# Kernel optimization log

Hardware: AMD Instinct MI355X
Metric: run time of the kernel (lower is better)

Reference implementation:

```python
import jax, jax.numpy as jnp
import numpy as np

N_NODES = 100000
N_EDGES = 1600000
N_GRAPHS = 128
IN_DIM, HID, OUT_DIM, DOC_DIM = 64, 128, 32, 768
LAYERS = 3


def setup_inputs() -> dict:
    key = jax.random.key(0)
    ks = jax.random.split(key, 24)
    s = 0.05
    inp = {
        "x": jax.random.normal(ks[0], (N_NODES, IN_DIM), jnp.float32),
        "doc_features": jax.random.normal(ks[1], (N_GRAPHS, DOC_DIM), jnp.float32),
        "edge_index": jax.random.randint(ks[2], (2, N_EDGES), 0, N_NODES, jnp.int64),
        "batch": jnp.sort(jax.random.randint(ks[3], (N_NODES,), 0, N_GRAPHS, jnp.int64)),
        # parameters (stored as [in, out] so y = x @ W + b)
        "node_w": jax.random.normal(ks[4], (IN_DIM, HID), jnp.float32) * s,
        "node_b": jnp.zeros((HID,), jnp.float32),
        "ggnn_w": jax.random.normal(ks[5], (LAYERS, HID, HID), jnp.float32) * s,
        "gru_w_ih": jax.random.normal(ks[6], (HID, 3 * HID), jnp.float32) * s,
        "gru_b_ih": jnp.zeros((3 * HID,), jnp.float32),
        "gru_w_hh": jax.random.normal(ks[7], (HID, 3 * HID), jnp.float32) * s,
        "gru_b_hh": jnp.zeros((3 * HID,), jnp.float32),
        "doc_w": jax.random.normal(ks[8], (DOC_DIM, HID), jnp.float32) * s,
        "doc_b": jnp.zeros((HID,), jnp.float32),
        "ln_g": jnp.ones((2 * HID,), jnp.float32),
        "ln_b": jnp.zeros((2 * HID,), jnp.float32),
        "fus_w": jax.random.normal(ks[9], (2 * HID, HID), jnp.float32) * s,
        "fus_b": jnp.zeros((HID,), jnp.float32),
        "task_w": jax.random.normal(ks[10], (HID, OUT_DIM), jnp.float32) * s,
        "task_b": jnp.zeros((OUT_DIM,), jnp.float32),
        "time_w": jax.random.normal(ks[11], (HID, 1), jnp.float32) * s,
        "time_b": jnp.zeros((1,), jnp.float32),
    }
    return inp


def _gru(m, h, w_ih, b_ih, w_hh, b_hh):
    gi = m @ w_ih + b_ih  # [N, 3H]
    gh = h @ w_hh + b_hh
    ir, iz, in_ = jnp.split(gi, 3, axis=-1)
    hr, hz, hn = jnp.split(gh, 3, axis=-1)
    r = jax.nn.sigmoid(ir + hr)
    z = jax.nn.sigmoid(iz + hz)
    n = jnp.tanh(in_ + r * hn)
    return (1.0 - z) * n + z * h


def reference(x, doc_features, node_w, node_b, ggnn_w, gru_w_ih, gru_b_ih,
              gru_w_hh, gru_b_hh, doc_w, doc_b, ln_g, ln_b, fus_w, fus_b,
              task_w, task_b, time_w, time_b, edge_index, batch):
    N = x.shape[0]
    src, dst = edge_index[0], edge_index[1]
    # node projection + ReLU
    h = jax.nn.relu(x @ node_w + node_b)  # [N, H]
    # GatedGraphConv: 3 layers of (linear -> scatter-add over edges -> GRU)
    for i in range(LAYERS):
        m = h @ ggnn_w[i]                              # [N, H]
        agg = jax.ops.segment_sum(m[src], dst, num_segments=N)  # scatter-add
        h = _gru(agg, h, gru_w_ih, gru_b_ih, gru_w_hh, gru_b_hh)
    # global mean pool over graphs
    sums = jax.ops.segment_sum(h, batch, num_segments=N_GRAPHS)  # [G, H]
    cnt = jax.ops.segment_sum(jnp.ones((N,), h.dtype), batch, num_segments=N_GRAPHS)
    pooled = sums / jnp.maximum(cnt, 1.0)[:, None]
    # doc projection + fusion head
    doc_emb = jax.nn.relu(doc_features @ doc_w + doc_b)  # [G, H]
    fusion = jnp.concatenate([pooled, doc_emb], axis=1)  # [G, 2H]
    mu = jnp.mean(fusion, axis=-1, keepdims=True)
    var = jnp.mean(jnp.square(fusion - mu), axis=-1, keepdims=True)
    fusion = (fusion - mu) * jax.lax.rsqrt(var + 1e-5) * ln_g + ln_b
    fusion = jax.nn.relu(fusion @ fus_w + fus_b)  # dropout is identity (eval)
    task_output = fusion @ task_w + task_b
    time_output = fusion @ time_w + time_b
    return (task_output, time_output)
```

## Files before the change

### kernel.cpp

```cpp
#include <hip/hip_runtime.h>

#define N_NODES  100000
#define N_EDGES  1600000
#define N_GRAPHS 128

#define BSH      8
#define BNODES   (1 << BSH)
#define NBUCK    391
#define NBLK_P1  512
#define EPB      (N_EDGES / NBLK_P1)
#define BKT_SCAN_N   (NBUCK * NBLK_P1)
#define SCAN_BLK_BKT 196
#define SCAN_BLK_NODE 98

typedef unsigned short u16;
typedef unsigned int   u32;
typedef __attribute__((ext_vector_type(8))) short short8;
typedef __attribute__((ext_vector_type(4))) float f32x4;

__device__ __forceinline__ float bf2f(u16 v) {
  union { u32 i; float f; } u; u.i = ((u32)v) << 16; return u.f;
}
__device__ __forceinline__ u16 f2bf(float f) {
  union { float f; u32 i; } u; u.f = f;
  u32 r = (u.i + 0x7fffu + ((u.i >> 16) & 1u)) >> 16;
  return (u16)r;
}
__device__ __forceinline__ float sigmoid_f(float x) { return 1.f / (1.f + __expf(-x)); }
__device__ __forceinline__ float tanh_f(float x) {
  x = fminf(15.f, fmaxf(-15.f, x));
  float e = __expf(2.f * x);
  return (e - 1.f) / (e + 1.f);
}
__device__ __forceinline__ int geti(const int* __restrict__ p, int i, int is64) {
  return p[is64 ? (2 * i) : i];
}

__global__ void detect_i64_kernel(const int* __restrict__ ei, const int* __restrict__ batch,
                                  int* __restrict__ flags) {
  int lane = threadIdx.x;
  {
    long long q = (long long)lane * (3200000 / 2 - 1) / 63;
    int pos = (int)(2 * q + 1);
    unsigned long long m = __ballot(ei[pos] != 0);
    if (lane == 0) flags[0] = (m == 0ull) ? 1 : 0;
  }
  {
    long long q = (long long)lane * (100000 / 2 - 1) / 63;
    int pos = (int)(2 * q + 1);
    unsigned long long m = __ballot(batch[pos] != 0);
    if (lane == 0) flags[1] = (m == 0ull) ? 1 : 0;
  }
}


__global__ __launch_bounds__(256)
void bucket_hist(const int* __restrict__ ei, const int* __restrict__ flags,
                 int* __restrict__ bcounts) {
  __shared__ int h[NBUCK];
  const int f = flags[0];
  for (int b = threadIdx.x; b < NBUCK; b += 256) h[b] = 0;
  __syncthreads();
  const int e0 = blockIdx.x * EPB;
  for (int i = threadIdx.x; i < EPB; i += 256) {
    int d = geti(ei, N_EDGES + e0 + i, f);
    atomicAdd(&h[d >> BSH], 1);
  }
  __syncthreads();
  for (int b = threadIdx.x; b < NBUCK; b += 256)
    bcounts[b * NBLK_P1 + blockIdx.x] = h[b];
}

__global__ __launch_bounds__(256)
void bucket_scatter(const int* __restrict__ ei, const int* __restrict__ flags,
                    const int* __restrict__ bbases, u32* __restrict__ bedges) {
  __shared__ int cur[NBUCK];
  const int f = flags[0];
  for (int b = threadIdx.x; b < NBUCK; b += 256)
    cur[b] = bbases[b * NBLK_P1 + blockIdx.x];
  __syncthreads();
  const int e0 = blockIdx.x * EPB;
  for (int i = threadIdx.x; i < EPB; i += 256) {
    int e = e0 + i;
    int d = geti(ei, N_EDGES + e, f);
    int s = geti(ei, e, f);
    int pos = atomicAdd(&cur[d >> BSH], 1);
    bedges[pos] = ((u32)(d & (BNODES - 1)) << 17) | (u32)s;
  }
}

__global__ __launch_bounds__(256)
void node_count(const u32* __restrict__ bedges, const int* __restrict__ bbases,
                int* __restrict__ counts) {
  __shared__ int h[BNODES];
  const int b = blockIdx.x;
  for (int i = threadIdx.x; i < BNODES; i += 256) h[i] = 0;
  __syncthreads();
  const int beg = bbases[b * NBLK_P1];
  const int end = (b + 1 < NBUCK) ? bbases[(b + 1) * NBLK_P1] : N_EDGES;
  for (int e = beg + threadIdx.x; e < end; e += 256)
    atomicAdd(&h[bedges[e] >> 17], 1);
  __syncthreads();
  const int node0 = b << BSH;
  for (int i = threadIdx.x; i < BNODES; i += 256)
    if (node0 + i < N_NODES) counts[node0 + i] = h[i];
}

__global__ __launch_bounds__(256)
void final_scatter(const u32* __restrict__ bedges, const int* __restrict__ bbases,
                   const int* __restrict__ offs, int* __restrict__ ssrc) {
  __shared__ int cur[BNODES];
  const int b = blockIdx.x;
  const int node0 = b << BSH;
  for (int i = threadIdx.x; i < BNODES; i += 256)
    cur[i] = (node0 + i < N_NODES) ? offs[node0 + i] : 0;
  __syncthreads();
  const int beg = bbases[b * NBLK_P1];
  const int end = (b + 1 < NBUCK) ? bbases[(b + 1) * NBLK_P1] : N_EDGES;
  for (int e = beg + threadIdx.x; e < end; e += 256) {
    u32 v = bedges[e];
    int pos = atomicAdd(&cur[v >> 17], 1);
    ssrc[pos] = (int)(v & 0x1FFFFu);
  }
}

__global__ __launch_bounds__(1024)
void scanA_kernel(const int* __restrict__ counts, int n, int* __restrict__ blocksums) {
  __shared__ int red[16];
  int i = blockIdx.x * 1024 + threadIdx.x;
  int v = (i < n) ? counts[i] : 0;
  for (int o = 32; o > 0; o >>= 1) v += __shfl_down(v, o, 64);
  int wv = threadIdx.x >> 6, lane = threadIdx.x & 63;
  if (lane == 0) red[wv] = v;
  __syncthreads();
  if (threadIdx.x < 16) {
    int s = red[threadIdx.x];
    for (int o = 8; o > 0; o >>= 1) s += __shfl_down(s, o, 64);
    if (threadIdx.x == 0) blocksums[blockIdx.x] = s;
  }
}

__global__ void scanB_kernel(const int* __restrict__ blocksums, int nblocks,
                             int* __restrict__ blockbase, int* __restrict__ total_out) {
  if (threadIdx.x == 0) {
    int run = 0;
    for (int b = 0; b < nblocks; ++b) { blockbase[b] = run; run += blocksums[b]; }
    if (total_out) *total_out = run;
  }
}

__global__ __launch_bounds__(1024)
void scanC_kernel(const int* __restrict__ counts, int n, const int* __restrict__ blockbase,
                  int* __restrict__ offsets) {
  __shared__ int buf[1024];
  int t = threadIdx.x;
  int i = blockIdx.x * 1024 + t;
  int v = (i < n) ? counts[i] : 0;
  buf[t] = v;
  __syncthreads();
  for (int o = 1; o < 1024; o <<= 1) {
    int add = (t >= o) ? buf[t - o] : 0;
    __syncthreads();
    buf[t] += add;
    __syncthreads();
  }
  if (i < n) offsets[i] = buf[t] - v + blockbase[blockIdx.x];
}

__global__ void transpose_kernel(const float* __restrict__ in, u16* __restrict__ out, int K, int N) {
  int i = blockIdx.x * 256 + threadIdx.x;
  if (i < K * N) {
    int k = i / N, n = i % N;
    out[n * K + k] = f2bf(in[i]);
  }
}

__global__ void wprime_kernel(const float* __restrict__ ggnn_w, const float* __restrict__ w_ih,
                              float* __restrict__ wp) {
  int i = blockIdx.x * 256 + threadIdx.x;
  if (i >= 3 * 128 * 384) return;
  int l = i / (128 * 384), r = i % (128 * 384), k = r / 384, c = r % 384;
  const float* W = ggnn_w + l * 128 * 128;
  float s = 0.f;
  for (int j = 0; j < 128; ++j) s += W[k * 128 + j] * w_ih[j * 384 + c];
  wp[i] = s;
}

__global__ void build_b2p_kernel(const float* __restrict__ wp, const float* __restrict__ w_hh,
                                 u16* __restrict__ b2p) {
  int g = blockIdx.x * 256 + threadIdx.x;
  if (g >= 8 * 1536 * 8) return;
  int e = g & 7;
  int grp = g >> 3;
  int ci = grp / 1536;
  int idx = grp % 1536;
  int n_lin = idx % 384;
  int ko = idx / 384;
  int k = ci * 32 + ko * 8 + e;
  float v = (k < 128) ? wp[k * 384 + n_lin] : w_hh[(k - 128) * 384 + n_lin];
  b2p[g] = f2bf(v);
}

__global__ __launch_bounds__(256)
void nodeproj_gemm(const float* __restrict__ A, const u16* __restrict__ BT,
                   const float* __restrict__ bias, u16* __restrict__ out, int M)
{
  constexpr int K_DIM = 64, N_DIM = 128, NT = 8, NCHUNK = 2;
  __shared__ u16 B_lds[N_DIM * 40];
  const int tid = threadIdx.x, lane = tid & 63, w = tid >> 6;
  const int strip = blockIdx.x * 64;
  const int ksub = (lane >> 4) * 8;
  union Frag { uint4 u; short8 s; };
  Frag af[NCHUNK];
  const int m_node = strip + w * 16 + (lane & 15);
  const bool avalid = (m_node < M);
#pragma unroll
  for (int ci = 0; ci < NCHUNK; ++ci) {
    int k0 = ci * 32 + ksub;
    short8 sv = {0,0,0,0,0,0,0,0};
    if (avalid) {
      const float* p = A + (size_t)m_node * K_DIM + k0;
      float4 f0 = *(const float4*)p;
      float4 f1 = *(const float4*)(p + 4);
      sv[0]=(short)f2bf(f0.x); sv[1]=(short)f2bf(f0.y); sv[2]=(short)f2bf(f0.z); sv[3]=(short)f2bf(f0.w);
      sv[4]=(short)f2bf(f1.x); sv[5]=(short)f2bf(f1.y); sv[6]=(short)f2bf(f1.z); sv[7]=(short)f2bf(f1.w);
    }
    af[ci].s = sv;
  }
  f32x4 acc[NT];
#pragma unroll
  for (int t = 0; t < NT; ++t) acc[t] = {0.f, 0.f, 0.f, 0.f};
  const int boff = (lane & 15) * 40 + ksub;
#pragma unroll
  for (int ci = 0; ci < NCHUNK; ++ci) {
    if (ci) __syncthreads();
    for (int g = tid; g < N_DIM * 4; g += 256) {
      int n = g >> 2, ko = g & 3;
      uint4 bv = *(const uint4*)(BT + (size_t)n * K_DIM + ci * 32 + ko * 8);
      *(uint4*)(&B_lds[n * 40 + ko * 8]) = bv;
    }
    __syncthreads();
    short8 a = af[ci].s;
#pragma unroll
    for (int t = 0; t < NT; ++t) {
      const short8 b = *(const short8*)(&B_lds[t * 16 * 40 + boff]);
      acc[t] = __builtin_amdgcn_mfma_f32_16x16x32_bf16(a, b, acc[t], 0, 0, 0);
    }
  }
  const int mrow = (lane >> 4) * 4;
#pragma unroll
  for (int t = 0; t < NT; ++t) {
    int col = t * 16 + (lane & 15);
    float bv = bias[col];
#pragma unroll
    for (int r = 0; r < 4; ++r) {
      int node = strip + w * 16 + mrow + r;
      if (node < M) out[(size_t)node * N_DIM + col] = f2bf(fmaxf(acc[t][r] + bv, 0.f));
    }
  }
}

__global__ __launch_bounds__(256)
void gru_gemm(const u16* __restrict__ agg, const u16* __restrict__ h,
              const u16* __restrict__ b2p, const float* __restrict__ b_ih,
              const float* __restrict__ b_hh, u16* __restrict__ hout, int M)
{
  __shared__ u16 Blds[24576];
  const int tid  = threadIdx.x;
  const int lane = tid & 63;
  const int w    = tid >> 6;
  const int bid  = blockIdx.x;
  const int linear = (bid & 7) * 391 + (bid >> 3);
  const int qc   = linear & 3;
  const int strip = (linear >> 2) * 128;
  const int lrow  = lane & 15;
  const int quad  = lane >> 4;
  const int ksub  = quad * 8;

  for (int idx = tid; idx < 3072; idx += 256) {
    const int run = idx >> 5, off = idx & 31;
    const int ci = run / 12, rem = run - ci * 12;
    const int qd = rem / 3, gate = rem - qd * 3;
    const size_t so = (size_t)ci * 12288 + qd * 3072 + gate * 1024 + qc * 256 + off * 8;
    *(uint4*)(&Blds[run * 256 + off * 8]) = *(const uint4*)(b2p + so);
  }

  f32x4 ar[2][2], az[2][2], ain[2][2], ahn[2][2];
#pragma unroll
  for (int s = 0; s < 2; ++s)
#pragma unroll
    for (int t = 0; t < 2; ++t) {
      ar[s][t] = {0.f,0.f,0.f,0.f}; az[s][t] = {0.f,0.f,0.f,0.f};
      ain[s][t] = {0.f,0.f,0.f,0.f}; ahn[s][t] = {0.f,0.f,0.f,0.f};
    }

  union Frag { uint4 u; short8 s8; };
  const int node0 = strip + w * 32 + lrow;
  const int node1 = node0 + 16;
  const bool v0 = (node0 < M), v1 = (node1 < M);

  Frag a0[2], a1[2];
  auto lda = [&](int ci, int p) {
    const u16* ap = (ci < 4) ? (agg + ci * 32 + ksub) : (h + (ci - 4) * 32 + ksub);
    uint4 z = {0u,0u,0u,0u};
    a0[p].u = v0 ? *(const uint4*)(ap + (size_t)node0 * 128) : z;
    a1[p].u = v1 ? *(const uint4*)(ap + (size_t)node1 * 128) : z;
  };

  lda(0, 0);
  lda(1, 1);
  __syncthreads();

#pragma unroll
  for (int ci = 0; ci < 8; ++ci) {
    const int p = ci & 1;
    const u16* lb = &Blds[ci * 3072 + quad * 768 + lrow * 8];
    short8 br0 = *(const short8*)(lb);
    short8 br1 = *(const short8*)(lb + 128);
    short8 bz0 = *(const short8*)(lb + 256);
    short8 bz1 = *(const short8*)(lb + 384);
    short8 bg0 = *(const short8*)(lb + 512);
    short8 bg1 = *(const short8*)(lb + 640);
    short8 A0 = a0[p].s8, A1 = a1[p].s8;
    if (ci < 6) lda(ci + 2, p);

    ar[0][0] = __builtin_amdgcn_mfma_f32_16x16x32_bf16(A0, br0, ar[0][0], 0, 0, 0);
    ar[1][0] = __builtin_amdgcn_mfma_f32_16x16x32_bf16(A1, br0, ar[1][0], 0, 0, 0);
    ar[0][1] = __builtin_amdgcn_mfma_f32_16x16x32_bf16(A0, br1, ar[0][1], 0, 0, 0);
    ar[1][1] = __builtin_amdgcn_mfma_f32_16x16x32_bf16(A1, br1, ar[1][1], 0, 0, 0);
    az[0][0] = __builtin_amdgcn_mfma_f32_16x16x32_bf16(A0, bz0, az[0][0], 0, 0, 0);
    az[1][0] = __builtin_amdgcn_mfma_f32_16x16x32_bf16(A1, bz0, az[1][0], 0, 0, 0);
    az[0][1] = __builtin_amdgcn_mfma_f32_16x16x32_bf16(A0, bz1, az[0][1], 0, 0, 0);
    az[1][1] = __builtin_amdgcn_mfma_f32_16x16x32_bf16(A1, bz1, az[1][1], 0, 0, 0);
    if (ci < 4) {
      ain[0][0] = __builtin_amdgcn_mfma_f32_16x16x32_bf16(A0, bg0, ain[0][0], 0, 0, 0);
      ain[1][0] = __builtin_amdgcn_mfma_f32_16x16x32_bf16(A1, bg0, ain[1][0], 0, 0, 0);
      ain[0][1] = __builtin_amdgcn_mfma_f32_16x16x32_bf16(A0, bg1, ain[0][1], 0, 0, 0);
      ain[1][1] = __builtin_amdgcn_mfma_f32_16x16x32_bf16(A1, bg1, ain[1][1], 0, 0, 0);
    } else {
      ahn[0][0] = __builtin_amdgcn_mfma_f32_16x16x32_bf16(A0, bg0, ahn[0][0], 0, 0, 0);
      ahn[1][0] = __builtin_amdgcn_mfma_f32_16x16x32_bf16(A1, bg0, ahn[1][0], 0, 0, 0);
      ahn[0][1] = __builtin_amdgcn_mfma_f32_16x16x32_bf16(A0, bg1, ahn[0][1], 0, 0, 0);
      ahn[1][1] = __builtin_amdgcn_mfma_f32_16x16x32_bf16(A1, bg1, ahn[1][1], 0, 0, 0);
    }
  }

#pragma unroll
  for (int t = 0; t < 2; ++t) {
    const int c = qc * 32 + t * 16 + lrow;
    const float brr = b_ih[c] + b_hh[c];
    const float bzz = b_ih[128 + c] + b_hh[128 + c];
    const float bin = b_ih[256 + c];
    const float bhn = b_hh[256 + c];
#pragma unroll
    for (int s = 0; s < 2; ++s) {
#pragma unroll
      for (int r = 0; r < 4; ++r) {
        const int nrow = strip + w * 32 + s * 16 + quad * 4 + r;
        if (nrow < M) {
          float rg = sigmoid_f(ar[s][t][r] + brr);
          float zg = sigmoid_f(az[s][t][r] + bzz);
          float hv = ahn[s][t][r] + bhn;
          float ng = tanh_f(ain[s][t][r] + bin + rg * hv);
          float hp = bf2f(h[(size_t)nrow * 128 + c]);
          hout[(size_t)nrow * 128 + c] = f2bf((1.f - zg) * ng + zg * hp);
        }
      }
    }
  }
}

__global__ __launch_bounds__(256)
void agg_kernel(const u16* __restrict__ m, const int* __restrict__ ssrc,
                const int* __restrict__ offsets, u16* __restrict__ agg)
{
  int node = blockIdx.x * 4 + (threadIdx.x >> 6);
  int lane = threadIdx.x & 63;
  if (node >= N_NODES) return;
  const int g = lane >> 4, l = lane & 15;
  int beg = offsets[node], end = offsets[node + 1];
  float s[8] = {0.f,0.f,0.f,0.f,0.f,0.f,0.f,0.f};
  for (int e = beg; e < end; e += 8) {
    uint4 v0 = {0u,0u,0u,0u}, v1 = {0u,0u,0u,0u};
    int e0 = e + g, e1 = e + 4 + g;
    if (e0 < end) { int src = ssrc[e0]; v0 = *(const uint4*)(m + (size_t)src * 128 + l * 8); }
    if (e1 < end) { int src = ssrc[e1]; v1 = *(const uint4*)(m + (size_t)src * 128 + l * 8); }
    u32 w0[4] = {v0.x, v0.y, v0.z, v0.w};
    u32 w1[4] = {v1.x, v1.y, v1.z, v1.w};
#pragma unroll
    for (int i = 0; i < 4; ++i) {
      s[2*i]   += bf2f((u16)(w0[i] & 0xffffu)) + bf2f((u16)(w1[i] & 0xffffu));
      s[2*i+1] += bf2f((u16)(w0[i] >> 16))     + bf2f((u16)(w1[i] >> 16));
    }
  }
#pragma unroll
  for (int i = 0; i < 8; ++i) {
    s[i] += __shfl_xor(s[i], 16, 64);
    s[i] += __shfl_xor(s[i], 32, 64);
  }
  if (g == 0) {
    uint4 o;
    o.x = (u32)f2bf(s[0]) | ((u32)f2bf(s[1]) << 16);
    o.y = (u32)f2bf(s[2]) | ((u32)f2bf(s[3]) << 16);
    o.z = (u32)f2bf(s[4]) | ((u32)f2bf(s[5]) << 16);
    o.w = (u32)f2bf(s[6]) | ((u32)f2bf(s[7]) << 16);
    *(uint4*)(agg + (size_t)node * 128 + l * 8) = o;
  }
}

__global__ __launch_bounds__(256)
void pool_kernel(const u16* __restrict__ h, const int* __restrict__ batch,
                 const int* __restrict__ flags, float* __restrict__ sums)
{
  const int c = threadIdx.x & 127;
  const int half = threadIdx.x >> 7;
  const int base = blockIdx.x * 128;
  const int f = flags[1];
  int gcur = -1; float s = 0.f;
  for (int i = half; i < 128; i += 2) {
    int n = base + i;
    if (n >= N_NODES) break;
    int g = geti(batch, n, f);
    if (g != gcur) {
      if (gcur >= 0) atomicAdd(&sums[gcur * 128 + c], s);
      s = 0.f; gcur = g;
    }
    s += bf2f(h[(size_t)n * 128 + c]);
  }
  if (gcur >= 0) atomicAdd(&sums[gcur * 128 + c], s);
}

__global__ __launch_bounds__(256)
void head2_kernel(const float* __restrict__ sums, const int* __restrict__ batch,
                  const int* __restrict__ flags,
                  const float* __restrict__ doc, const float* __restrict__ doc_w, const float* __restrict__ doc_b,
                  const float* __restrict__ ln_g, const float* __restrict__ ln_b,
                  const float* __restrict__ fus_w, const float* __restrict__ fus_b,
                  const float* __restrict__ task_w, const float* __restrict__ task_b,
                  const float* __restrict__ time_w, const float* __restrict__ time_b,
                  float* __restrict__ out_task, float* __restrict__ out_time)
{
  const int g = blockIdx.x;
  const int t = threadIdx.x;
  __shared__ float fusion[256];
  __shared__ float fh[128];
  __shared__ float dpart[256];
  __shared__ int seg[2];

  if (t < 2) {
    int f = flags[1];
    int target = g + t, lo = 0, hi = N_NODES;
    while (lo < hi) { int mid = (lo + hi) >> 1; if (geti(batch, mid, f) < target) lo = mid + 1; else hi = mid; }
    seg[t] = lo;
  }
  {
    int c = t & 127, kh = t >> 7;
    float s = 0.f;
    for (int k = kh * 384; k < kh * 384 + 384; ++k) s += doc[g * 768 + k] * doc_w[k * 128 + c];
    dpart[t] = s;
  }
  __syncthreads();

  if (t < 128) {
    float cnt = (float)(seg[1] - seg[0]);
    fusion[t] = sums[g * 128 + t] / fmaxf(cnt, 1.f);
  } else {
    int c = t - 128;
    fusion[t] = fmaxf(dpart[c] + dpart[c + 128] + doc_b[c], 0.f);
  }
  __syncthreads();

  float mu = 0.f;
  for (int i = 0; i < 256; ++i) mu += fusion[i];
  mu *= (1.f / 256.f);
  float var = 0.f;
  for (int i = 0; i < 256; ++i) { float d = fusion[i] - mu; var += d * d; }
  var *= (1.f / 256.f);
  float inv = rsqrtf(var + 1e-5f);
  float norm = (fusion[t] - mu) * inv * ln_g[t] + ln_b[t];
  __syncthreads();
  fusion[t] = norm;
  __syncthreads();

  if (t < 128) {
    float s = 0.f;
    for (int k = 0; k < 256; ++k) s += fusion[k] * fus_w[k * 128 + t];
    s += fus_b[t];
    fh[t] = fmaxf(s, 0.f);
  }
  __syncthreads();

  if (t < 32) {
    float s = 0.f;
    for (int k = 0; k < 128; ++k) s += fh[k] * task_w[k * 32 + t];
    s += task_b[t];
    out_task[g * 32 + t] = s;
  }
  if (t == 32) {
    float s = 0.f;
    for (int k = 0; k < 128; ++k) s += fh[k] * time_w[k];
    s += time_b[0];
    out_time[g] = s;
  }
}

extern "C" void kernel_launch(void* const* d_in, const int* in_sizes, int n_in,
                              void* d_out, int out_size, void* d_ws, size_t ws_size,
                              hipStream_t stream)
{
  const float* x        = (const float*)d_in[0];
  const float* doc      = (const float*)d_in[1];
  const int*   ei       = (const int*)d_in[2];
  const int*   batch    = (const int*)d_in[3];
  const float* node_w   = (const float*)d_in[4];
  const float* node_b   = (const float*)d_in[5];
  const float* ggnn_w   = (const float*)d_in[6];
  const float* gru_w_ih = (const float*)d_in[7];
  const float* gru_b_ih = (const float*)d_in[8];
  const float* gru_w_hh = (const float*)d_in[9];
  const float* gru_b_hh = (const float*)d_in[10];
  const float* doc_w    = (const float*)d_in[11];
  const float* doc_b    = (const float*)d_in[12];
  const float* ln_g     = (const float*)d_in[13];
  const float* ln_b     = (const float*)d_in[14];
  const float* fus_w    = (const float*)d_in[15];
  const float* fus_b    = (const float*)d_in[16];
  const float* task_w   = (const float*)d_in[17];
  const float* task_b   = (const float*)d_in[18];
  const float* time_w   = (const float*)d_in[19];
  const float* time_b   = (const float*)d_in[20];

  char* ws = (char*)d_ws;
  size_t off = 0;
  auto alloc = [&](size_t bytes) -> void* {
    void* p = ws + off;
    off = (off + bytes + 255) & ~(size_t)255;
    return p;
  };
  u16* aggb    = (u16*)alloc((size_t)N_NODES * 128 * 2);
  u16* hA      = (u16*)alloc((size_t)N_NODES * 128 * 2);
  u16* hB      = (u16*)alloc((size_t)N_NODES * 128 * 2);
  u16* nwT     = (u16*)alloc(64 * 128 * 2);
  u16* b2p     = (u16*)alloc(3 * 8 * 1536 * 8 * 2);
  float* wp    = (float*)alloc(3 * 128 * 384 * 4);
  float* sums  = (float*)alloc(N_GRAPHS * 128 * 4);
  int* counts  = (int*)alloc((size_t)N_NODES * 4);
  int* offs    = (int*)alloc((size_t)(N_NODES + 1) * 4);
  int* ssrc    = (int*)alloc((size_t)N_EDGES * 4);
  int* bsum    = (int*)alloc(SCAN_BLK_BKT * 4);
  int* bbase   = (int*)alloc(SCAN_BLK_BKT * 4);
  int* flags   = (int*)alloc(2 * 4);

  u32* bedges  = (u32*)aggb;
  int* bcounts = (int*)((char*)aggb + 6400000);
  int* bbases  = (int*)((char*)aggb + 7200768);

  hipMemsetAsync(sums, 0, (size_t)N_GRAPHS * 128 * 4, stream);

  detect_i64_kernel<<<1, 64, 0, stream>>>(ei, batch, flags);

  bucket_hist<<<NBLK_P1, 256, 0, stream>>>(ei, flags, bcounts);
  scanA_kernel<<<SCAN_BLK_BKT, 1024, 0, stream>>>(bcounts, BKT_SCAN_N, bsum);
  scanB_kernel<<<1, 64, 0, stream>>>(bsum, SCAN_BLK_BKT, bbase, (int*)nullptr);
  scanC_kernel<<<SCAN_BLK_BKT, 1024, 0, stream>>>(bcounts, BKT_SCAN_N, bbase, bbases);
  bucket_scatter<<<NBLK_P1, 256, 0, stream>>>(ei, flags, bbases, bedges);
  node_count<<<NBUCK, 256, 0, stream>>>(bedges, bbases, counts);
  scanA_kernel<<<SCAN_BLK_NODE, 1024, 0, stream>>>(counts, N_NODES, bsum);
  scanB_kernel<<<1, 64, 0, stream>>>(bsum, SCAN_BLK_NODE, bbase, offs + N_NODES);
  scanC_kernel<<<SCAN_BLK_NODE, 1024, 0, stream>>>(counts, N_NODES, bbase, offs);
  final_scatter<<<NBUCK, 256, 0, stream>>>(bedges, bbases, offs, ssrc);

  transpose_kernel<<<(64 * 128 + 255) / 256, 256, 0, stream>>>(node_w, nwT, 64, 128);
  wprime_kernel<<<(3 * 128 * 384 + 255) / 256, 256, 0, stream>>>(ggnn_w, gru_w_ih, wp);
  for (int l = 0; l < 3; ++l)
    build_b2p_kernel<<<(8 * 1536 * 8 + 255) / 256, 256, 0, stream>>>(
        wp + l * 128 * 384, gru_w_hh, b2p + (size_t)l * 8 * 1536 * 8);

  const int GB = (N_NODES + 63) / 64;
  const int GBGRU = ((N_NODES + 127) / 128) * 4;
  nodeproj_gemm<<<GB, 256, 0, stream>>>(x, nwT, node_b, hA, N_NODES);

  u16* hcur = hA;
  u16* hnext = hB;
  for (int l = 0; l < 3; ++l) {
    agg_kernel<<<(N_NODES + 3) / 4, 256, 0, stream>>>(hcur, ssrc, offs, aggb);
    gru_gemm<<<GBGRU, 256, 0, stream>>>(aggb, hcur, b2p + (size_t)l * 8 * 1536 * 8,
                                        gru_b_ih, gru_b_hh, hnext, N_NODES);
    u16* tmp = hcur; hcur = hnext; hnext = tmp;
  }

  pool_kernel<<<(N_NODES + 127) / 128, 256, 0, stream>>>(hcur, batch, flags, sums);

  float* out_task = (float*)d_out;
  float* out_time = out_task + N_GRAPHS * 32;
  head2_kernel<<<N_GRAPHS, 256, 0, stream>>>(sums, batch, flags, doc, doc_w, doc_b, ln_g, ln_b,
                                             fus_w, fus_b, task_w, task_b, time_w, time_b,
                                             out_task, out_time);
}
```

Before: 639.0 us.

## Retile GRU GEMM to 64-node by 16-column tiles with smaller LDS

The GRU gemm now gives each block 64 nodes and 16 output columns, across 8 column groups, instead of 128 nodes and 32 columns. The weights are repacked into a new per-column-group layout, and only half of the K range (6 KB) is staged in LDS at a time, with a mid-loop reload. The goal is to cut LDS and register use so that 8 blocks fit per CU, raising occupancy and latency hiding. The cost is that each A fragment is reused less (one MFMA row tile instead of two), the A loads are repeated across 8 column blocks instead of 4, and there are extra barriers.

```diff
diff --git a/kernel.cpp b/kernel.cpp
--- a/kernel.cpp
+++ b/kernel.cpp
@@ -186,19 +186,22 @@
   wp[i] = s;
 }
 
-__global__ void build_b2p_kernel(const float* __restrict__ wp, const float* __restrict__ w_hh,
-                                 u16* __restrict__ b2p) {
+__global__ void build_b2q_kernel(const float* __restrict__ wp, const float* __restrict__ w_hh,
+                                 u16* __restrict__ b2q) {
   int g = blockIdx.x * 256 + threadIdx.x;
-  if (g >= 8 * 1536 * 8) return;
-  int e = g & 7;
-  int grp = g >> 3;
-  int ci = grp / 1536;
-  int idx = grp % 1536;
-  int n_lin = idx % 384;
-  int ko = idx / 384;
-  int k = ci * 32 + ko * 8 + e;
+  if (g >= 98304) return;
+  int r = g;
+  int e    = r & 7;  r >>= 3;
+  int quad = r & 3;  r >>= 2;
+  int col  = r & 15; r >>= 4;
+  int gate = r % 3;  r /= 3;
+  int ci4  = r & 3;  r >>= 2;
+  int half = r & 1;  r >>= 1;
+  int oc   = r;
+  int k = half * 128 + ci4 * 32 + quad * 8 + e;
+  int n_lin = gate * 128 + oc * 16 + col;
   float v = (k < 128) ? wp[k * 384 + n_lin] : w_hh[(k - 128) * 384 + n_lin];
-  b2p[g] = f2bf(v);
+  b2q[g] = f2bf(v);
 }
 
 __global__ __launch_bounds__(256)
@@ -260,112 +263,81 @@
   }
 }
 
-__global__ __launch_bounds__(256)
+__global__ __launch_bounds__(256, 8)
 void gru_gemm(const u16* __restrict__ agg, const u16* __restrict__ h,
-              const u16* __restrict__ b2p, const float* __restrict__ b_ih,
+              const u16* __restrict__ b2q, const float* __restrict__ b_ih,
               const float* __restrict__ b_hh, u16* __restrict__ hout, int M)
 {
-  __shared__ u16 Blds[24576];
+  __shared__ u16 Blds[6144];
   const int tid  = threadIdx.x;
   const int lane = tid & 63;
   const int w    = tid >> 6;
   const int bid  = blockIdx.x;
-  const int linear = (bid & 7) * 391 + (bid >> 3);
-  const int qc   = linear & 3;
-  const int strip = (linear >> 2) * 128;
-  const int lrow  = lane & 15;
-  const int quad  = lane >> 4;
-  const int ksub  = quad * 8;
-
-  for (int idx = tid; idx < 3072; idx += 256) {
-    const int run = idx >> 5, off = idx & 31;
-    const int ci = run / 12, rem = run - ci * 12;
-    const int qd = rem / 3, gate = rem - qd * 3;
-    const size_t so = (size_t)ci * 12288 + qd * 3072 + gate * 1024 + qc * 256 + off * 8;
-    *(uint4*)(&Blds[run * 256 + off * 8]) = *(const uint4*)(b2p + so);
-  }
-
-  f32x4 ar[2][2], az[2][2], ain[2][2], ahn[2][2];
-#pragma unroll
-  for (int s = 0; s < 2; ++s)
-#pragma unroll
-    for (int t = 0; t < 2; ++t) {
-      ar[s][t] = {0.f,0.f,0.f,0.f}; az[s][t] = {0.f,0.f,0.f,0.f};
-      ain[s][t] = {0.f,0.f,0.f,0.f}; ahn[s][t] = {0.f,0.f,0.f,0.f};
-    }
+  const int linear = (bid & 7) * 1563 + (bid >> 3);
+  const int oc   = linear & 7;
+  const int strip = (linear >> 3) * 64;
+  const int lrow = lane & 15;
+  const int quad = lane >> 4;
+
+  const int node = strip + w * 16 + lrow;
+  const bool nv = (node < M);
+  const u16* qsrc = b2q + (size_t)oc * 12288;
 
   union Frag { uint4 u; short8 s8; };
-  const int node0 = strip + w * 32 + lrow;
-  const int node1 = node0 + 16;
-  const bool v0 = (node0 < M), v1 = (node1 < M);
-
-  Frag a0[2], a1[2];
+  Frag a[2];
+  const uint4 zz = {0u, 0u, 0u, 0u};
   auto lda = [&](int ci, int p) {
-    const u16* ap = (ci < 4) ? (agg + ci * 32 + ksub) : (h + (ci - 4) * 32 + ksub);
-    uint4 z = {0u,0u,0u,0u};
-    a0[p].u = v0 ? *(const uint4*)(ap + (size_t)node0 * 128) : z;
-    a1[p].u = v1 ? *(const uint4*)(ap + (size_t)node1 * 128) : z;
+    const u16* ap = (ci < 4) ? (agg + ci * 32 + quad * 8) : (h + (ci - 4) * 32 + quad * 8);
+    a[p].u = nv ? *(const uint4*)(ap + (size_t)node * 128) : zz;
   };
 
   lda(0, 0);
   lda(1, 1);
+  for (int idx = tid; idx < 768; idx += 256)
+    *(uint4*)(&Blds[idx * 8]) = *(const uint4*)(qsrc + idx * 8);
+
+  f32x4 ar = {0.f,0.f,0.f,0.f}, az = {0.f,0.f,0.f,0.f};
+  f32x4 ain = {0.f,0.f,0.f,0.f}, ahn = {0.f,0.f,0.f,0.f};
+
   __syncthreads();
 
 #pragma unroll
   for (int ci = 0; ci < 8; ++ci) {
+    if (ci == 4) {
+      __syncthreads();
+      for (int idx = tid; idx < 768; idx += 256)
+        *(uint4*)(&Blds[idx * 8]) = *(const uint4*)(qsrc + 6144 + idx * 8);
+      __syncthreads();
+    }
     const int p = ci & 1;
-    const u16* lb = &Blds[ci * 3072 + quad * 768 + lrow * 8];
-    short8 br0 = *(const short8*)(lb);
-    short8 br1 = *(const short8*)(lb + 128);
-    short8 bz0 = *(const short8*)(lb + 256);
-    short8 bz1 = *(const short8*)(lb + 384);
-    short8 bg0 = *(const short8*)(lb + 512);
-    short8 bg1 = *(const short8*)(lb + 640);
-    short8 A0 = a0[p].s8, A1 = a1[p].s8;
+    const u16* lb = &Blds[(ci & 3) * 1536 + lrow * 32 + quad * 8];
+    short8 br = *(const short8*)(lb);
+    short8 bz = *(const short8*)(lb + 512);
+    short8 bg = *(const short8*)(lb + 1024);
+    short8 A = a[p].s8;
     if (ci < 6) lda(ci + 2, p);
 
-    ar[0][0] = __builtin_amdgcn_mfma_f32_16x16x32_bf16(A0, br0, ar[0][0], 0, 0, 0);
-    ar[1][0] = __builtin_amdgcn_mfma_f32_16x16x32_bf16(A1, br0, ar[1][0], 0, 0, 0);
-    ar[0][1] = __builtin_amdgcn_mfma_f32_16x16x32_bf16(A0, br1, ar[0][1], 0, 0, 0);
-    ar[1][1] = __builtin_amdgcn_mfma_f32_16x16x32_bf16(A1, br1, ar[1][1], 0, 0, 0);
-    az[0][0] = __builtin_amdgcn_mfma_f32_16x16x32_bf16(A0, bz0, az[0][0], 0, 0, 0);
-    az[1][0] = __builtin_amdgcn_mfma_f32_16x16x32_bf16(A1, bz0, az[1][0], 0, 0, 0);
-    az[0][1] = __builtin_amdgcn_mfma_f32_16x16x32_bf16(A0, bz1, az[0][1], 0, 0, 0);
-    az[1][1] = __builtin_amdgcn_mfma_f32_16x16x32_bf16(A1, bz1, az[1][1], 0, 0, 0);
-    if (ci < 4) {
-      ain[0][0] = __builtin_amdgcn_mfma_f32_16x16x32_bf16(A0, bg0, ain[0][0], 0, 0, 0);
-      ain[1][0] = __builtin_amdgcn_mfma_f32_16x16x32_bf16(A1, bg0, ain[1][0], 0, 0, 0);
-      ain[0][1] = __builtin_amdgcn_mfma_f32_16x16x32_bf16(A0, bg1, ain[0][1], 0, 0, 0);
-      ain[1][1] = __builtin_amdgcn_mfma_f32_16x16x32_bf16(A1, bg1, ain[1][1], 0, 0, 0);
-    } else {
-      ahn[0][0] = __builtin_amdgcn_mfma_f32_16x16x32_bf16(A0, bg0, ahn[0][0], 0, 0, 0);
-      ahn[1][0] = __builtin_amdgcn_mfma_f32_16x16x32_bf16(A1, bg0, ahn[1][0], 0, 0, 0);
-      ahn[0][1] = __builtin_amdgcn_mfma_f32_16x16x32_bf16(A0, bg1, ahn[0][1], 0, 0, 0);
-      ahn[1][1] = __builtin_amdgcn_mfma_f32_16x16x32_bf16(A1, bg1, ahn[1][1], 0, 0, 0);
-    }
-  }
-
-#pragma unroll
-  for (int t = 0; t < 2; ++t) {
-    const int c = qc * 32 + t * 16 + lrow;
-    const float brr = b_ih[c] + b_hh[c];
-    const float bzz = b_ih[128 + c] + b_hh[128 + c];
-    const float bin = b_ih[256 + c];
-    const float bhn = b_hh[256 + c];
-#pragma unroll
-    for (int s = 0; s < 2; ++s) {
-#pragma unroll
-      for (int r = 0; r < 4; ++r) {
-        const int nrow = strip + w * 32 + s * 16 + quad * 4 + r;
-        if (nrow < M) {
-          float rg = sigmoid_f(ar[s][t][r] + brr);
-          float zg = sigmoid_f(az[s][t][r] + bzz);
-          float hv = ahn[s][t][r] + bhn;
-          float ng = tanh_f(ain[s][t][r] + bin + rg * hv);
-          float hp = bf2f(h[(size_t)nrow * 128 + c]);
-          hout[(size_t)nrow * 128 + c] = f2bf((1.f - zg) * ng + zg * hp);
-        }
-      }
+    ar = __builtin_amdgcn_mfma_f32_16x16x32_bf16(A, br, ar, 0, 0, 0);
+    az = __builtin_amdgcn_mfma_f32_16x16x32_bf16(A, bz, az, 0, 0, 0);
+    if (ci < 4) ain = __builtin_amdgcn_mfma_f32_16x16x32_bf16(A, bg, ain, 0, 0, 0);
+    else        ahn = __builtin_amdgcn_mfma_f32_16x16x32_bf16(A, bg, ahn, 0, 0, 0);
+  }
+
+  const int c = oc * 16 + lrow;
+  const float brr = b_ih[c] + b_hh[c];
+  const float bzz = b_ih[128 + c] + b_hh[128 + c];
+  const float bin = b_ih[256 + c];
+  const float bhn = b_hh[256 + c];
+#pragma unroll
+  for (int r = 0; r < 4; ++r) {
+    const int nrow = strip + w * 16 + quad * 4 + r;
+    if (nrow < M) {
+      float rg = sigmoid_f(ar[r] + brr);
+      float zg = sigmoid_f(az[r] + bzz);
+      float hv = ahn[r] + bhn;
+      float ng = tanh_f(ain[r] + bin + rg * hv);
+      float hp = bf2f(h[(size_t)nrow * 128 + c]);
+      hout[(size_t)nrow * 128 + c] = f2bf((1.f - zg) * ng + zg * hp);
     }
   }
 }
@@ -541,7 +513,7 @@
   u16* hA      = (u16*)alloc((size_t)N_NODES * 128 * 2);
   u16* hB      = (u16*)alloc((size_t)N_NODES * 128 * 2);
   u16* nwT     = (u16*)alloc(64 * 128 * 2);
-  u16* b2p     = (u16*)alloc(3 * 8 * 1536 * 8 * 2);
+  u16* b2q     = (u16*)alloc(3 * 98304 * 2);
   float* wp    = (float*)alloc(3 * 128 * 384 * 4);
   float* sums  = (float*)alloc(N_GRAPHS * 128 * 4);
   int* counts  = (int*)alloc((size_t)N_NODES * 4);
@@ -573,18 +545,18 @@
   transpose_kernel<<<(64 * 128 + 255) / 256, 256, 0, stream>>>(node_w, nwT, 64, 128);
   wprime_kernel<<<(3 * 128 * 384 + 255) / 256, 256, 0, stream>>>(ggnn_w, gru_w_ih, wp);
   for (int l = 0; l < 3; ++l)
-    build_b2p_kernel<<<(8 * 1536 * 8 + 255) / 256, 256, 0, stream>>>(
-        wp + l * 128 * 384, gru_w_hh, b2p + (size_t)l * 8 * 1536 * 8);
+    build_b2q_kernel<<<(98304 + 255) / 256, 256, 0, stream>>>(
+        wp + l * 128 * 384, gru_w_hh, b2q + (size_t)l * 98304);
 
   const int GB = (N_NODES + 63) / 64;
-  const int GBGRU = ((N_NODES + 127) / 128) * 4;
+  const int GBGRU = ((N_NODES + 63) / 64) * 8;
   nodeproj_gemm<<<GB, 256, 0, stream>>>(x, nwT, node_b, hA, N_NODES);
 
   u16* hcur = hA;
   u16* hnext = hB;
   for (int l = 0; l < 3; ++l) {
     agg_kernel<<<(N_NODES + 3) / 4, 256, 0, stream>>>(hcur, ssrc, offs, aggb);
-    gru_gemm<<<GBGRU, 256, 0, stream>>>(aggb, hcur, b2p + (size_t)l * 8 * 1536 * 8,
+    gru_gemm<<<GBGRU, 256, 0, stream>>>(aggb, hcur, b2q + (size_t)l * 98304,
                                         gru_b_ih, gru_b_hh, hnext, N_NODES);
     u16* tmp = hcur; hcur = hnext; hnext = tmp;
   }
```

Result: slower. 672.1 us (+5.2%).
